# Kernel tuning notes

Hardware: AMD Instinct MI355X
Metric: run time of the kernel (lower is better)

## Reference

```python
import jax, jax.numpy as jnp
import numpy as np

N_NODES = 100000
N_EDGES = 3200000
F_IN = 512
HID = 16
N_CLS = 16


def setup_inputs() -> dict:
    key = jax.random.key(0)
    ks = jax.random.split(key, 6)
    x = jax.random.normal(ks[0], (N_NODES, F_IN), dtype=jnp.float32)
    edge_index = jax.random.randint(ks[1], (2, N_EDGES), 0, N_NODES, dtype=jnp.int64)
    lin1_w = jax.random.normal(ks[2], (HID, F_IN), dtype=jnp.float32) * (1.0 / np.sqrt(F_IN))
    lin1_b = jnp.zeros((HID,), jnp.float32)
    lin2_w = jax.random.normal(ks[3], (N_CLS, HID), dtype=jnp.float32) * (1.0 / np.sqrt(HID))
    lin2_b = jnp.zeros((N_CLS,), jnp.float32)
    beta2 = jnp.ones((1,), jnp.float32)
    return {"x": x, "edge_index": edge_index, "lin1_w": lin1_w, "lin1_b": lin1_b,
            "lin2_w": lin2_w, "lin2_b": lin2_b, "beta2": beta2}


def _agnn_prop(h, src, dst, beta, n_nodes):
    # h: [N, D]; src/dst: [E'] (self-loops included)
    hn = h / jnp.maximum(jnp.linalg.norm(h, axis=-1, keepdims=True), 1e-12)
    # cosine similarity per edge, scaled by beta
    alpha = beta * jnp.sum(hn[src] * hn[dst], axis=-1)  # [E']
    # segment softmax over incoming edges of each dst node
    a_max = jax.ops.segment_max(alpha, dst, num_segments=n_nodes)
    a_exp = jnp.exp(alpha - a_max[dst])
    a_sum = jax.ops.segment_sum(a_exp, dst, num_segments=n_nodes)
    w = a_exp / a_sum[dst]
    # weighted scatter-aggregate of source features
    return jax.ops.segment_sum(h[src] * w[:, None], dst, num_segments=n_nodes)


def reference(x, edge_index, lin1_w, lin1_b, lin2_w, lin2_b, beta2):
    n = x.shape[0]
    # eval mode: dropout is identity
    h = jax.nn.relu(x @ lin1_w.T + lin1_b)  # [N, 16]
    # add self-loops (PyG AGNNConv default)
    loop = jnp.arange(n, dtype=edge_index.dtype)
    src = jnp.concatenate([edge_index[0], loop])
    dst = jnp.concatenate([edge_index[1], loop])
    h = _agnn_prop(h, src, dst, jnp.float32(1.0), n)      # prop1: fixed beta=1
    h = _agnn_prop(h, src, dst, beta2[0], n)               # prop2: learnable beta
    logits = h @ lin2_w.T + lin2_b
    return jax.nn.log_softmax(logits, axis=1)
```

## Files before the change

kernel.cpp:

```cpp
#include <hip/hip_runtime.h>
#include <hip/hip_bf16.h>

#define F_IN 512
#define NB 128
#define SRC_BITS 17
#define SRC_MASK ((1 << SRC_BITS) - 1)
#define T_APP 16384
#define GPAD 16
#define CAP 4736
#define LOG2E 1.4426950408889634f

typedef unsigned int uint;

__device__ __forceinline__ uint f2bf(float f) {
  uint u = __float_as_uint(f);
  return (u + 0x7fffu + ((u >> 16) & 1u)) >> 16;
}
__device__ __forceinline__ float bflo(uint u) { return __uint_as_float(u << 16); }
__device__ __forceinline__ float bfhi(uint u) { return __uint_as_float(u & 0xffff0000u); }

__device__ __forceinline__ void lin1_body(
    const float* __restrict__ x, const float* __restrict__ w1,
    const float* __restrict__ b1, uint* __restrict__ h0b,
    int N, int nodeBase, char* smem) {
  float* sW = (float*)smem;
  for (int i = threadIdx.x; i < 16 * F_IN / 4; i += 512)
    ((float4*)sW)[i] = ((const float4*)w1)[i];
  __syncthreads();

  int wave = threadIdx.x >> 6;
  int lane = threadIdx.x & 63;
  int j = lane & 15;
  int g = lane >> 4;
  int node = nodeBase + wave * 4 + g;
  if (node >= N) return;

  const float4* xr = (const float4*)(x + (size_t)node * F_IN);
  float acc[16];
#pragma unroll
  for (int k = 0; k < 16; ++k) acc[k] = 0.f;

#pragma unroll
  for (int t = 0; t < 8; ++t) {
    float4 xv = xr[t * 16 + j];
#pragma unroll
    for (int k = 0; k < 16; ++k) {
      float4 wv = *(const float4*)&sW[k * F_IN + t * 64 + j * 4];
      acc[k] = fmaf(xv.x, wv.x, fmaf(xv.y, wv.y, fmaf(xv.z, wv.z, fmaf(xv.w, wv.w, acc[k]))));
    }
  }
#pragma unroll
  for (int s = 1; s < 16; s <<= 1) {
#pragma unroll
    for (int k = 0; k < 16; ++k) acc[k] += __shfl_xor(acc[k], s, 64);
  }
  float hv = 0.f;
#pragma unroll
  for (int k = 0; k < 16; ++k)
    if (j == k) hv = acc[k];
  hv += b1[j];
  hv = fmaxf(hv, 0.f);

  float hp = __shfl_xor(hv, 1, 64);
  if (!(j & 1))
    h0b[(size_t)node * 8 + (j >> 1)] = f2bf(hv) | (f2bf(hp) << 16);
}

__global__ __launch_bounds__(512) void bzero_kernel(int* __restrict__ p, int n) {
  int i = blockIdx.x * 512 + threadIdx.x;
  if (i < n) p[i] = 0;
}

__global__ __launch_bounds__(512) void fa_append_lin1(
    const int* __restrict__ src, const int* __restrict__ dst,
    int* __restrict__ cur, int* __restrict__ elist, int E, int nb,
    const float* __restrict__ x, const float* __restrict__ w1,
    const float* __restrict__ b1, uint* __restrict__ h0b,
    int N, int appBlocks, int nodeBase) {
  __shared__ __align__(16) char smem[32768];
  if (blockIdx.x < appBlocks) {
    int* hist = (int*)smem;
    int* base = hist + 1024;
    int* curl = base + 1024;
    int t = threadIdx.x;
    int e0 = blockIdx.x * T_APP;
    int e1 = min(E, e0 + T_APP);
    for (int i = t; i < nb; i += 512) hist[i] = 0;
    __syncthreads();
    for (int i = e0 + t; i < e1; i += 512) atomicAdd(&hist[dst[i] >> 7], 1);
    __syncthreads();
    for (int i = t; i < nb; i += 512) {
      int c = hist[i];
      base[i] = c ? atomicAdd(&cur[i * GPAD], c) : 0;
      curl[i] = 0;
    }
    __syncthreads();
    for (int i = e0 + t; i < e1; i += 512) {
      int d = dst[i];
      int b = d >> 7;
      int slot = base[b] + atomicAdd(&curl[b], 1);
      elist[(size_t)b * CAP + slot] = src[i] | ((d & (NB - 1)) << SRC_BITS);
    }
  } else {
    lin1_body(x, w1, b1, h0b, N, nodeBase + (blockIdx.x - appBlocks) * 32, smem);
  }
}

__global__ __launch_bounds__(512) void fb_sort_lin1(
    const int* __restrict__ elist, const int* __restrict__ cur,
    int* __restrict__ csr, int* __restrict__ offg, int* __restrict__ degg,
    const float* __restrict__ x, const float* __restrict__ w1,
    const float* __restrict__ b1, uint* __restrict__ h0b,
    int N, int sortBlocks, int nodeBase) {
  __shared__ __align__(16) char smem[32768];
  if (blockIdx.x < sortBlocks) {
    int* hist = (int*)smem;
    int* scn = hist + NB;
    int* curw = scn + NB;
    int b = blockIdx.x, t = threadIdx.x;
    size_t base = (size_t)b * CAP;
    int cnt = cur[b * GPAD];
    int node0 = b * NB, nn = min(NB, N - node0);
    if (t < NB) hist[t] = 0;
    __syncthreads();
    for (int i = t; i < cnt; i += 512) atomicAdd(&hist[elist[base + i] >> SRC_BITS], 1);
    __syncthreads();
    if (t < NB) scn[t] = hist[t];
    __syncthreads();
    for (int st = 1; st < NB; st <<= 1) {
      int v = (t >= st && t < NB) ? scn[t - st] : 0;
      __syncthreads();
      if (t < NB) scn[t] += v;
      __syncthreads();
    }
    if (t < NB) {
      int ex = scn[t] - hist[t];
      curw[t] = ex;
      if (t < nn) {
        offg[node0 + t] = (int)(base + ex);
        degg[node0 + t] = hist[t];
      }
    }
    __syncthreads();
    for (int i = t; i < cnt; i += 512) {
      int pk = elist[base + i];
      int ld = pk >> SRC_BITS;
      int slot = atomicAdd(&curw[ld], 1);
      csr[base + slot] = pk & SRC_MASK;
    }
  } else {
    lin1_body(x, w1, b1, h0b, N, nodeBase + (blockIdx.x - sortBlocks) * 32, smem);
  }
}

template <bool LAST>
__global__ __launch_bounds__(256) void prop_kernel(
    const uint2* __restrict__ hb, const int* __restrict__ off,
    const int* __restrict__ degg, const int* __restrict__ csr,
    const float* __restrict__ beta_ptr, uint2* __restrict__ houtb,
    const float* __restrict__ w2, const float* __restrict__ b2,
    float* __restrict__ out, int N) {
  __shared__ float sw2t[256];
  __shared__ float sb2c[16];
  __shared__ float so[16][16];
  if (LAST) {
    if (threadIdx.x < 256) {
      int c = threadIdx.x & 15, m = threadIdx.x >> 4;
      sw2t[m * 16 + c] = w2[c * 16 + m];
    }
    if (threadIdx.x < 16) sb2c[threadIdx.x] = b2[threadIdx.x];
    __syncthreads();
  }

  int wv = threadIdx.x >> 6;
  int lane = threadIdx.x & 63;
  int q = lane >> 4;
  int l4 = lane & 15;
  int p = l4 & 3;
  int slot = l4 >> 2;
  int d = blockIdx.x * 16 + wv * 4 + q;
  if (!LAST && d >= N) return;
  int dc = min(d, N - 1);

  float beta = beta_ptr ? beta_ptr[0] : 1.0f;
  uint2 hdu = hb[(size_t)dc * 4 + p];
  float hd0 = bflo(hdu.x), hd1 = bfhi(hdu.x), hd2 = bflo(hdu.y), hd3 = bfhi(hdu.y);

  float ssd = fmaf(hd0, hd0, fmaf(hd1, hd1, fmaf(hd2, hd2, hd3 * hd3)));
  ssd += __shfl_xor(ssd, 1, 64);
  ssd += __shfl_xor(ssd, 2, 64);
  float rnd = rsqrtf(fmaxf(ssd, 1e-24f));
  float brnl2d = beta * LOG2E * rnd;

  float den = 0.f, n0 = 0.f, n1 = 0.f, n2 = 0.f, n3 = 0.f;
  if (slot == 0) {
    float es = exp2f(beta * LOG2E);
    den = es;
    n0 = es * hd0; n1 = es * hd1; n2 = es * hd2; n3 = es * hd3;
  }

  int base = off[dc];
  int dg = degg[dc];
  for (int i = slot; i < dg; i += 8) {
    int i1 = i + 4;
    bool v1 = i1 < dg;
    int s0 = csr[base + i];
    int s1 = v1 ? csr[base + i1] : s0;
    uint2 au = hb[(size_t)s0 * 4 + p];
    uint2 bu = hb[(size_t)s1 * 4 + p];
    float a0 = bflo(au.x), a1 = bfhi(au.x), a2 = bflo(au.y), a3 = bfhi(au.y);
    float c0 = bflo(bu.x), c1 = bfhi(bu.x), c2 = bflo(bu.y), c3 = bfhi(bu.y);
    float dt0 = fmaf(a0, hd0, fmaf(a1, hd1, fmaf(a2, hd2, a3 * hd3)));
    float dt1 = fmaf(c0, hd0, fmaf(c1, hd1, fmaf(c2, hd2, c3 * hd3)));
    float ss0 = fmaf(a0, a0, fmaf(a1, a1, fmaf(a2, a2, a3 * a3)));
    float ss1 = fmaf(c0, c0, fmaf(c1, c1, fmaf(c2, c2, c3 * c3)));
    dt0 += __shfl_xor(dt0, 1, 64);
    dt1 += __shfl_xor(dt1, 1, 64);
    ss0 += __shfl_xor(ss0, 1, 64);
    ss1 += __shfl_xor(ss1, 1, 64);
    dt0 += __shfl_xor(dt0, 2, 64);
    dt1 += __shfl_xor(dt1, 2, 64);
    ss0 += __shfl_xor(ss0, 2, 64);
    ss1 += __shfl_xor(ss1, 2, 64);
    float rs0 = rsqrtf(fmaxf(ss0, 1e-24f));
    float rs1 = rsqrtf(fmaxf(ss1, 1e-24f));
    float e0 = exp2f(dt0 * rs0 * brnl2d);
    float e1 = exp2f(dt1 * rs1 * brnl2d);
    e1 = v1 ? e1 : 0.f;
    den += e0 + e1;
    n0 = fmaf(e1, c0, fmaf(e0, a0, n0));
    n1 = fmaf(e1, c1, fmaf(e0, a1, n1));
    n2 = fmaf(e1, c2, fmaf(e0, a2, n2));
    n3 = fmaf(e1, c3, fmaf(e0, a3, n3));
  }
#pragma unroll
  for (int st = 4; st < 16; st <<= 1) {
    den += __shfl_xor(den, st, 64);
    n0 += __shfl_xor(n0, st, 64);
    n1 += __shfl_xor(n1, st, 64);
    n2 += __shfl_xor(n2, st, 64);
    n3 += __shfl_xor(n3, st, 64);
  }
  float inv = 1.f / den;
  float o0 = n0 * inv, o1 = n1 * inv, o2 = n2 * inv, o3 = n3 * inv;

  if (!LAST) {
    if (slot == 0) {
      uint2 w;
      w.x = f2bf(o0) | (f2bf(o1) << 16);
      w.y = f2bf(o2) | (f2bf(o3) << 16);
      houtb[(size_t)d * 4 + p] = w;
    }
  } else {
    int row = wv * 4 + q;
    if (slot == 0) {
      so[row][4 * p + 0] = o0;
      so[row][4 * p + 1] = o1;
      so[row][4 * p + 2] = o2;
      so[row][4 * p + 3] = o3;
    }
    __syncthreads();
    {
      int node = threadIdx.x >> 4;
      int c = threadIdx.x & 15;
      int dd = blockIdx.x * 16 + node;
      float lg = sb2c[c];
#pragma unroll
      for (int m = 0; m < 16; ++m)
        lg = fmaf(so[node][m], sw2t[m * 16 + c], lg);
      float mx = lg;
      mx = fmaxf(mx, __shfl_xor(mx, 1, 64));
      mx = fmaxf(mx, __shfl_xor(mx, 2, 64));
      mx = fmaxf(mx, __shfl_xor(mx, 4, 64));
      mx = fmaxf(mx, __shfl_xor(mx, 8, 64));
      float ex = __expf(lg - mx);
      float sm = ex;
      sm += __shfl_xor(sm, 1, 64);
      sm += __shfl_xor(sm, 2, 64);
      sm += __shfl_xor(sm, 4, 64);
      sm += __shfl_xor(sm, 8, 64);
      if (dd < N) out[(size_t)dd * 16 + c] = lg - mx - logf(sm);
    }
  }
}

extern "C" void kernel_launch(void* const* d_in, const int* in_sizes, int n_in,
                              void* d_out, int out_size, void* d_ws, size_t ws_size,
                              hipStream_t stream) {
  const float* x     = (const float*)d_in[0];
  const int*   ei    = (const int*)d_in[1];
  const float* w1    = (const float*)d_in[2];
  const float* b1    = (const float*)d_in[3];
  const float* w2    = (const float*)d_in[4];
  const float* b2    = (const float*)d_in[5];
  const float* beta2 = (const float*)d_in[6];
  float* out = (float*)d_out;

  const int N = in_sizes[0] / F_IN;
  const int E = in_sizes[1] / 2;
  const int* src = ei;
  const int* dst = ei + E;
  const int nb = (N + NB - 1) / NB;
  const int appBlocks = (E + T_APP - 1) / T_APP;

  const int linBlocks = (N + 31) / 32;
  const int lc0 = linBlocks / 2;
  const int lc1 = linBlocks - lc0;
  const int nb0 = 0, nb1 = lc0 * 32;

  char* ws = (char*)d_ws;
  size_t wo = 0;
  auto take = [&](size_t bytes) -> void* {
    void* p = ws + wo;
    wo = (wo + bytes + 255) & ~(size_t)255;
    return p;
  };
  int*   cur   = (int*)take((size_t)nb * GPAD * 4);
  int*   offg  = (int*)take((size_t)N * 4);
  int*   degg  = (int*)take((size_t)N * 4);
  int*   csr   = (int*)take((size_t)nb * CAP * 4);
  int*   elist = (int*)take((size_t)nb * CAP * 4);
  uint*  h0b   = (uint*)take((size_t)N * 8 * 4);
  uint*  h1b   = (uint*)(elist);

  bzero_kernel<<<(nb * GPAD + 511) / 512, 512, 0, stream>>>(cur, nb * GPAD);
  fa_append_lin1<<<appBlocks + lc0, 512, 0, stream>>>(
      src, dst, cur, elist, E, nb, x, w1, b1, h0b, N, appBlocks, nb0);
  fb_sort_lin1<<<nb + lc1, 512, 0, stream>>>(
      elist, cur, csr, offg, degg, x, w1, b1, h0b, N, nb, nb1);

  prop_kernel<false><<<(N + 15) / 16, 256, 0, stream>>>(
      (const uint2*)h0b, offg, degg, csr, nullptr, (uint2*)h1b,
      nullptr, nullptr, nullptr, N);
  prop_kernel<true><<<(N + 15) / 16, 256, 0, stream>>>(
      (const uint2*)h1b, offg, degg, csr, beta2, nullptr, w2, b2, out, N);
}
```

Measured before the change: 185.7 us.

## Compute lin1 with bf16 MFMA 16x16x32 instead of scalar FMA reductions

Rewrites the first linear layer so each wave computes a 16-node by 16-output tile with bf16 MFMA instructions, replacing per-lane fp32 FMAs and a shuffle-reduction tree. Weights are pre-swizzled into bf16 fragment layout in shared memory, and each block now covers 128 nodes instead of 32, so fewer lin1 blocks are launched. Inputs are rounded to bf16 before the multiply, which lowers precision of the hidden activations (they were already stored as bf16). The lin1 part is bound by reading x from memory, so the gain comes mainly from less ALU and shuffle work.

```diff
diff --git a/kernel.cpp b/kernel.cpp
--- a/kernel.cpp
+++ b/kernel.cpp
@@ -11,6 +11,8 @@
 #define LOG2E 1.4426950408889634f
 
 typedef unsigned int uint;
+typedef __attribute__((ext_vector_type(8))) short bfrag8;
+typedef __attribute__((ext_vector_type(4))) float ffrag4;
 
 __device__ __forceinline__ uint f2bf(float f) {
   uint u = __float_as_uint(f);
@@ -23,47 +25,51 @@
     const float* __restrict__ x, const float* __restrict__ w1,
     const float* __restrict__ b1, uint* __restrict__ h0b,
     int N, int nodeBase, char* smem) {
-  float* sW = (float*)smem;
-  for (int i = threadIdx.x; i < 16 * F_IN / 4; i += 512)
-    ((float4*)sW)[i] = ((const float4*)w1)[i];
+  uint* sWB = (uint*)smem;
+  for (int idx = threadIdx.x; idx < 4096; idx += 512) {
+    int s = idx >> 8, lane = (idx >> 2) & 63, i = idx & 3;
+    int j = lane & 15;
+    int k = s * 32 + ((lane >> 4) << 3) + (i << 1);
+    sWB[idx] = f2bf(w1[j * F_IN + k]) | (f2bf(w1[j * F_IN + k + 1]) << 16);
+  }
   __syncthreads();
 
-  int wave = threadIdx.x >> 6;
+  int wv = threadIdx.x >> 6;
   int lane = threadIdx.x & 63;
   int j = lane & 15;
-  int g = lane >> 4;
-  int node = nodeBase + wave * 4 + g;
-  if (node >= N) return;
-
-  const float4* xr = (const float4*)(x + (size_t)node * F_IN);
-  float acc[16];
+  int ko = lane >> 4;
+  int node0 = nodeBase + wv * 16;
+  if (node0 >= N) return;
+  int rowc = min(node0 + j, N - 1);
+  const float4* xr = (const float4*)(x + (size_t)rowc * F_IN) + ko * 2;
+
+  ffrag4 acc = {0.f, 0.f, 0.f, 0.f};
 #pragma unroll
-  for (int k = 0; k < 16; ++k) acc[k] = 0.f;
-
+  for (int s = 0; s < 16; ++s) {
+    float4 xa = xr[s * 8];
+    float4 xb = xr[s * 8 + 1];
+    bfrag8 a;
+    a[0] = (short)f2bf(xa.x); a[1] = (short)f2bf(xa.y);
+    a[2] = (short)f2bf(xa.z); a[3] = (short)f2bf(xa.w);
+    a[4] = (short)f2bf(xb.x); a[5] = (short)f2bf(xb.y);
+    a[6] = (short)f2bf(xb.z); a[7] = (short)f2bf(xb.w);
+    uint4 bu = *(uint4*)&sWB[(s * 64 + lane) * 4];
+    bfrag8 b;
+    b[0] = (short)(bu.x & 0xffff); b[1] = (short)(bu.x >> 16);
+    b[2] = (short)(bu.y & 0xffff); b[3] = (short)(bu.y >> 16);
+    b[4] = (short)(bu.z & 0xffff); b[5] = (short)(bu.z >> 16);
+    b[6] = (short)(bu.w & 0xffff); b[7] = (short)(bu.w >> 16);
+    acc = __builtin_amdgcn_mfma_f32_16x16x32_bf16(a, b, acc, 0, 0, 0);
+  }
+  float b1j = b1[j];
 #pragma unroll
-  for (int t = 0; t < 8; ++t) {
-    float4 xv = xr[t * 16 + j];
-#pragma unroll
-    for (int k = 0; k < 16; ++k) {
-      float4 wv = *(const float4*)&sW[k * F_IN + t * 64 + j * 4];
-      acc[k] = fmaf(xv.x, wv.x, fmaf(xv.y, wv.y, fmaf(xv.z, wv.z, fmaf(xv.w, wv.w, acc[k]))));
-    }
-  }
-#pragma unroll
-  for (int s = 1; s < 16; s <<= 1) {
-#pragma unroll
-    for (int k = 0; k < 16; ++k) acc[k] += __shfl_xor(acc[k], s, 64);
-  }
-  float hv = 0.f;
-#pragma unroll
-  for (int k = 0; k < 16; ++k)
-    if (j == k) hv = acc[k];
-  hv += b1[j];
-  hv = fmaxf(hv, 0.f);
-
-  float hp = __shfl_xor(hv, 1, 64);
-  if (!(j & 1))
-    h0b[(size_t)node * 8 + (j >> 1)] = f2bf(hv) | (f2bf(hp) << 16);
+  for (int r = 0; r < 4; ++r) {
+    float hv = fmaxf(acc[r] + b1j, 0.f);
+    float hp = __shfl_xor(hv, 1, 64);
+    int node = node0 + ko * 4 + r;
+    if (!(j & 1) && node < N)
+      h0b[(size_t)node * 8 + (j >> 1)] = f2bf(hv) | (f2bf(hp) << 16);
+  }
 }
 
 __global__ __launch_bounds__(512) void bzero_kernel(int* __restrict__ p, int n) {
@@ -102,7 +108,7 @@
       elist[(size_t)b * CAP + slot] = src[i] | ((d & (NB - 1)) << SRC_BITS);
     }
   } else {
-    lin1_body(x, w1, b1, h0b, N, nodeBase + (blockIdx.x - appBlocks) * 32, smem);
+    lin1_body(x, w1, b1, h0b, N, nodeBase + (blockIdx.x - appBlocks) * 128, smem);
   }
 }
 
@@ -149,7 +155,7 @@
       csr[base + slot] = pk & SRC_MASK;
     }
   } else {
-    lin1_body(x, w1, b1, h0b, N, nodeBase + (blockIdx.x - sortBlocks) * 32, smem);
+    lin1_body(x, w1, b1, h0b, N, nodeBase + (blockIdx.x - sortBlocks) * 128, smem);
   }
 }
 
@@ -303,10 +309,10 @@
   const int nb = (N + NB - 1) / NB;
   const int appBlocks = (E + T_APP - 1) / T_APP;
 
-  const int linBlocks = (N + 31) / 32;
+  const int linBlocks = (N + 127) / 128;
   const int lc0 = linBlocks / 2;
   const int lc1 = linBlocks - lc0;
-  const int nb0 = 0, nb1 = lc0 * 32;
+  const int nb0 = 0, nb1 = lc0 * 128;
 
   char* ws = (char*)d_ws;
   size_t wo = 0;
```

New measurement: 182.6 us. About the same (-1.7%).
